# Performance work log

Hardware: AMD Instinct MI355X
Metric: run time of the kernel (lower is better)

Reference implementation:

```python
import jax, jax.numpy as jnp
import numpy as np


def setup_inputs() -> dict:
    key = jax.random.key(0)
    k1, k2 = jax.random.split(key)
    # x: (batch=16, channels=256, window=64, n_patches=128)
    x = jax.random.normal(k1, (16, 256, 64, 128), dtype=jnp.float32)
    # codebooks: (nsubq=4, codebook_size=2**(num_bits//2)=256, sub_channels=64)
    codebooks = jax.random.normal(k2, (4, 256, 64), dtype=jnp.float32)
    return {"x": x, "codebooks": codebooks}


def reference(x, codebooks):
    B, C, W, P = x.shape
    ns, K, sc = codebooks.shape  # ns=4, K=256, sc=C//ns
    # split channels into nsubq subspaces: (B, ns, sc, W, P) -> (ns, B*W*P, sc)
    xs = x.reshape(B, ns, sc, W, P).transpose(1, 0, 3, 4, 2).reshape(ns, B * W * P, sc)
    # squared euclidean distances (argmin identical to cdist argmin)
    d2 = (jnp.sum(xs * xs, axis=-1, keepdims=True)
          - 2.0 * jnp.einsum('snc,skc->snk', xs, codebooks)
          + jnp.sum(codebooks * codebooks, axis=-1)[:, None, :])  # (ns, N, K)
    idx = jnp.argmin(d2, axis=-1)  # (ns, N)
    q = jnp.take_along_axis(codebooks, idx[:, :, None], axis=1)  # (ns, N, sc)
    # faithful to the torch code: data was flattened in (B, W, P) order but
    # view()'d back as (B, P, W) -- reshape reproduces that reinterpretation
    q = q.reshape(ns, B, P, W, sc).transpose(1, 2, 3, 0, 4).reshape(B, P, W, C)
    # final permute(0, 3, 2, 1) -> (B, C, W, P)
    return q.transpose(0, 3, 2, 1)
```

## Files before the change

### kernel.cpp

```cpp
#include <hip/hip_runtime.h>

#define NSQ 4
#define KCB 256
#define SCH 64
#define NVEC (16*64*128)

__global__ void pq_norms(const float* __restrict__ cb, float* __restrict__ cn)
{
    const int s = blockIdx.x, k = threadIdx.x;
    const float* row = cb + (size_t)(s * KCB + k) * SCH;
    float n = 0.f;
#pragma unroll
    for (int j4 = 0; j4 < 16; ++j4) {
        float4 v = *(const float4*)(row + j4 * 4);
        n = fmaf(v.x, v.x, n); n = fmaf(v.y, v.y, n);
        n = fmaf(v.z, v.z, n); n = fmaf(v.w, v.w, n);
    }
    cn[s * KCB + k] = n;
}

__global__ __launch_bounds__(512, 2) void pq_pass1(const float* __restrict__ x,
                                                   const float* __restrict__ cb,
                                                   const float* __restrict__ cnorm,
                                                   int* __restrict__ idx_out)
{
    __shared__ float cbt[64][256];
    const int tid = threadIdx.x;
    const int s   = blockIdx.x >> 7;
    const int blk = blockIdx.x & 127;
    const int tk  = tid & 15;
    const int tn  = tid >> 4;
    const int swz = ((tk ^ (tk >> 2)) & 3) << 2;

    if (tid < 256) {
        const int k    = tid;
        const int tks  = k >> 4;
        const int szs  = ((tks ^ (tks >> 2)) & 3) << 2;
        const int col  = (k & ~15) | ((k & 15) ^ szs);
        const float* row = cb + (size_t)(s * KCB + k) * SCH;
#pragma unroll
        for (int j4 = 0; j4 < 16; ++j4) {
            float4 v = *(const float4*)(row + j4 * 4);
            cbt[j4*4 + 0][col] = v.x;
            cbt[j4*4 + 1][col] = v.y;
            cbt[j4*4 + 2][col] = v.z;
            cbt[j4*4 + 3][col] = v.w;
        }
    }
    __syncthreads();

    const int cb0 = (tk << 4) | (0  ^ swz);
    const int cb1 = (tk << 4) | (4  ^ swz);
    const int cb2 = (tk << 4) | (8  ^ swz);
    const int cb3 = (tk << 4) | (12 ^ swz);
    const float* cnp = cnorm + s * KCB + (tk << 4);

    int n_base = blk * 1024;
    const float* xp = x + ((size_t)(((n_base >> 13) * 256 + s * 64) * 64 +
                                    ((n_base >> 7) & 63))) * 128 + 4 * tn;
    float4 xv = *(const float4*)xp;

    for (int t = 0; t < 8; ++t) {
        float acc[4][16];
#pragma unroll
        for (int nn = 0; nn < 4; ++nn)
#pragma unroll
            for (int kk = 0; kk < 16; ++kk) acc[nn][kk] = 0.f;

#pragma unroll 2
        for (int j = 0; j < 63; ++j) {
            float4 xn = *(const float4*)(xp + (size_t)(j + 1) * 8192);
            float c[16];
            {
                float4 t0 = *(const float4*)&cbt[j][cb0];
                float4 t1 = *(const float4*)&cbt[j][cb1];
                float4 t2 = *(const float4*)&cbt[j][cb2];
                float4 t3 = *(const float4*)&cbt[j][cb3];
                c[0]=t0.x; c[1]=t0.y; c[2]=t0.z; c[3]=t0.w;
                c[4]=t1.x; c[5]=t1.y; c[6]=t1.z; c[7]=t1.w;
                c[8]=t2.x; c[9]=t2.y; c[10]=t2.z; c[11]=t2.w;
                c[12]=t3.x; c[13]=t3.y; c[14]=t3.z; c[15]=t3.w;
            }
#pragma unroll
            for (int kk = 0; kk < 16; ++kk) {
                acc[0][kk] = fmaf(xv.x, c[kk], acc[0][kk]);
                acc[1][kk] = fmaf(xv.y, c[kk], acc[1][kk]);
                acc[2][kk] = fmaf(xv.z, c[kk], acc[2][kk]);
                acc[3][kk] = fmaf(xv.w, c[kk], acc[3][kk]);
            }
            xv = xn;
        }
        {
            const int nb2 = blk * 1024 + (t < 7 ? (t + 1) : t) * 128;
            const float* xp2 = x + ((size_t)(((nb2 >> 13) * 256 + s * 64) * 64 +
                                             ((nb2 >> 7) & 63))) * 128 + 4 * tn;
            float4 xnext = *(const float4*)xp2;

            float c[16];
            {
                float4 t0 = *(const float4*)&cbt[63][cb0];
                float4 t1 = *(const float4*)&cbt[63][cb1];
                float4 t2 = *(const float4*)&cbt[63][cb2];
                float4 t3 = *(const float4*)&cbt[63][cb3];
                c[0]=t0.x; c[1]=t0.y; c[2]=t0.z; c[3]=t0.w;
                c[4]=t1.x; c[5]=t1.y; c[6]=t1.z; c[7]=t1.w;
                c[8]=t2.x; c[9]=t2.y; c[10]=t2.z; c[11]=t2.w;
                c[12]=t3.x; c[13]=t3.y; c[14]=t3.z; c[15]=t3.w;
            }
#pragma unroll
            for (int kk = 0; kk < 16; ++kk) {
                acc[0][kk] = fmaf(xv.x, c[kk], acc[0][kk]);
                acc[1][kk] = fmaf(xv.y, c[kk], acc[1][kk]);
                acc[2][kk] = fmaf(xv.z, c[kk], acc[2][kk]);
                acc[3][kk] = fmaf(xv.w, c[kk], acc[3][kk]);
            }
            xv = xnext;
            xp = xp2;
        }

        float best[4] = {3.4e38f, 3.4e38f, 3.4e38f, 3.4e38f};
        int   bidx[4] = {0, 0, 0, 0};
#pragma unroll
        for (int kk = 0; kk < 16; ++kk) {
            const float cn = cnp[kk];
            const int k = (tk << 4) + kk;
#pragma unroll
            for (int nn = 0; nn < 4; ++nn) {
                float d = fmaf(-2.f, acc[nn][kk], cn);
                bool better = (d < best[nn]);
                best[nn] = better ? d : best[nn];
                bidx[nn] = better ? k : bidx[nn];
            }
        }
#pragma unroll
        for (int m = 8; m; m >>= 1) {
#pragma unroll
            for (int nn = 0; nn < 4; ++nn) {
                float ob = __shfl_xor(best[nn], m, 64);
                int   oi = __shfl_xor(bidx[nn], m, 64);
                bool take = (ob < best[nn]) || (ob == best[nn] && oi < bidx[nn]);
                best[nn] = take ? ob : best[nn];
                bidx[nn] = take ? oi : bidx[nn];
            }
        }
        if (tk == 0) {
            int4 r; r.x = bidx[0]; r.y = bidx[1]; r.z = bidx[2]; r.w = bidx[3];
            *(int4*)(idx_out + (size_t)s * NVEC + n_base + 4 * tn) = r;
        }
        n_base += 128;
    }
}

__global__ __launch_bounds__(256) void pq_pass2(const float* __restrict__ cb,
                                                const int* __restrict__ idx,
                                                float* __restrict__ out)
{
    __shared__ int   L[64][65];
    __shared__ float cbs[256][9];
    const int tid = threadIdx.x;
    const int bid = blockIdx.x;
    const int jq  = bid & 7;
    const int ph  = (bid >> 3) & 1;
    const int s   = (bid >> 4) & 3;
    const int b   = bid >> 6;
    const int p0  = ph * 64;
    const int j0  = jq * 8;

    const int* ip = idx + (size_t)s * NVEC + b * 8192 + p0 * 64;
#pragma unroll
    for (int it = 0; it < 16; ++it) {
        int g = it * 256 + tid;
        L[g & 63][g >> 6] = ip[g];
    }
    const float* cp = cb + (size_t)s * (KCB * SCH) + j0;
#pragma unroll
    for (int it = 0; it < 2; ++it) {
        int t = it * 256 + tid;
        int k = t >> 1, jj4 = (t & 1) * 4;
        float4 v = *(const float4*)(cp + (size_t)k * SCH + jj4);
        cbs[k][jj4 + 0] = v.x; cbs[k][jj4 + 1] = v.y;
        cbs[k][jj4 + 2] = v.z; cbs[k][jj4 + 3] = v.w;
    }
    __syncthreads();

    int kv[4][4];
#pragma unroll
    for (int q = 0; q < 4; ++q) {
        int ch = q * 256 + tid;
        int w  = ch >> 4, pp = (ch & 15) * 4;
#pragma unroll
        for (int e = 0; e < 4; ++e) kv[q][e] = L[w][pp + e];
    }

#pragma unroll
    for (int cc = 0; cc < 8; ++cc) {
        const int c = s * 64 + j0 + cc;
        float* op = out + ((size_t)(b * 256 + c) * 64) * 128 + p0;
#pragma unroll
        for (int q = 0; q < 4; ++q) {
            int ch = q * 256 + tid;
            int w  = ch >> 4, pp = (ch & 15) * 4;
            float4 v;
            v.x = cbs[kv[q][0]][cc];
            v.y = cbs[kv[q][1]][cc];
            v.z = cbs[kv[q][2]][cc];
            v.w = cbs[kv[q][3]][cc];
            *(float4*)(op + (size_t)w * 128 + pp) = v;
        }
    }
}

extern "C" void kernel_launch(void* const* d_in, const int* in_sizes, int n_in,
                              void* d_out, int out_size, void* d_ws, size_t ws_size,
                              hipStream_t stream) {
    (void)in_sizes; (void)n_in; (void)out_size; (void)ws_size;
    const float* x   = (const float*)d_in[0];
    const float* cbk = (const float*)d_in[1];
    float*       out = (float*)d_out;
    int*         idx = (int*)d_ws;
    float*       cnrm = (float*)d_out;

    pq_norms<<<NSQ, KCB, 0, stream>>>(cbk, cnrm);
    pq_pass1<<<NSQ * 128, 512, 0, stream>>>(x, cbk, cnrm, idx);
    pq_pass2<<<16 * NSQ * 2 * 8, 256, 0, stream>>>(cbk, idx, out);
}
```

Measured before the change: 545.3 us.

## Split pass1 into many small blocks with chunked codebook staging in LDS

The distance kernel moves from 512 persistent-style blocks, each covering 1024 vectors with the full 64x256 codebook in LDS, to 8192 blocks of 256 threads covering 64 vectors each. The codebook is now staged in four 16-row chunks separated by barriers, so LDS per block drops from 64 KB to 16 KB and more blocks can be resident per CU. The goal is better occupancy and load balance across the GPU. In exchange, every block reloads the whole codebook from global or L2 memory and pays extra barriers, and the amortization of codebook staging across 8 tiles is lost.

```diff
diff --git a/kernel.cpp b/kernel.cpp
--- a/kernel.cpp
+++ b/kernel.cpp
@@ -19,35 +19,29 @@
     cn[s * KCB + k] = n;
 }
 
-__global__ __launch_bounds__(512, 2) void pq_pass1(const float* __restrict__ x,
+__global__ __launch_bounds__(256, 4) void pq_pass1(const float* __restrict__ x,
                                                    const float* __restrict__ cb,
                                                    const float* __restrict__ cnorm,
                                                    int* __restrict__ idx_out)
 {
-    __shared__ float cbt[64][256];
-    const int tid = threadIdx.x;
-    const int s   = blockIdx.x >> 7;
-    const int blk = blockIdx.x & 127;
-    const int tk  = tid & 15;
-    const int tn  = tid >> 4;
-    const int swz = ((tk ^ (tk >> 2)) & 3) << 2;
-
-    if (tid < 256) {
-        const int k    = tid;
-        const int tks  = k >> 4;
-        const int szs  = ((tks ^ (tks >> 2)) & 3) << 2;
-        const int col  = (k & ~15) | ((k & 15) ^ szs);
-        const float* row = cb + (size_t)(s * KCB + k) * SCH;
-#pragma unroll
-        for (int j4 = 0; j4 < 16; ++j4) {
-            float4 v = *(const float4*)(row + j4 * 4);
-            cbt[j4*4 + 0][col] = v.x;
-            cbt[j4*4 + 1][col] = v.y;
-            cbt[j4*4 + 2][col] = v.z;
-            cbt[j4*4 + 3][col] = v.w;
-        }
-    }
-    __syncthreads();
+    __shared__ float cbt[16][256];
+    const int tid  = threadIdx.x;
+    const int s    = blockIdx.x >> 11;
+    const int blkn = blockIdx.x & 2047;
+    const int tk   = tid & 15;
+    const int tn   = tid >> 4;
+    const int swz  = ((tk ^ (tk >> 2)) & 3) << 2;
+
+    const int n_base = blkn * 64;
+    const int b   = n_base >> 13;
+    const int w   = (n_base >> 7) & 63;
+    const int p0  = n_base & 127;
+
+    const int k    = tid;
+    const int tks  = k >> 4;
+    const int szs  = ((tks ^ (tks >> 2)) & 3) << 2;
+    const int col  = (k & ~15) | ((k & 15) ^ szs);
+    const float* cbrow = cb + (size_t)(s * KCB + k) * SCH;
 
     const int cb0 = (tk << 4) | (0  ^ swz);
     const int cb1 = (tk << 4) | (4  ^ swz);
@@ -55,27 +49,41 @@
     const int cb3 = (tk << 4) | (12 ^ swz);
     const float* cnp = cnorm + s * KCB + (tk << 4);
 
-    int n_base = blk * 1024;
-    const float* xp = x + ((size_t)(((n_base >> 13) * 256 + s * 64) * 64 +
-                                    ((n_base >> 7) & 63))) * 128 + 4 * tn;
+    const float* xp = x + ((size_t)((b * 256 + s * 64) * 64 + w)) * 128 + p0 + 4 * tn;
     float4 xv = *(const float4*)xp;
 
-    for (int t = 0; t < 8; ++t) {
-        float acc[4][16];
-#pragma unroll
-        for (int nn = 0; nn < 4; ++nn)
-#pragma unroll
-            for (int kk = 0; kk < 16; ++kk) acc[nn][kk] = 0.f;
-
-#pragma unroll 2
-        for (int j = 0; j < 63; ++j) {
-            float4 xn = *(const float4*)(xp + (size_t)(j + 1) * 8192);
+    float acc[4][16];
+#pragma unroll
+    for (int nn = 0; nn < 4; ++nn)
+#pragma unroll
+        for (int kk = 0; kk < 16; ++kk) acc[nn][kk] = 0.f;
+
+    for (int ch = 0; ch < 4; ++ch) {
+        __syncthreads();
+        {
+            const float* rp = cbrow + ch * 16;
+            float4 v0 = *(const float4*)(rp + 0);
+            float4 v1 = *(const float4*)(rp + 4);
+            float4 v2 = *(const float4*)(rp + 8);
+            float4 v3 = *(const float4*)(rp + 12);
+            cbt[ 0][col] = v0.x; cbt[ 1][col] = v0.y; cbt[ 2][col] = v0.z; cbt[ 3][col] = v0.w;
+            cbt[ 4][col] = v1.x; cbt[ 5][col] = v1.y; cbt[ 6][col] = v1.z; cbt[ 7][col] = v1.w;
+            cbt[ 8][col] = v2.x; cbt[ 9][col] = v2.y; cbt[10][col] = v2.z; cbt[11][col] = v2.w;
+            cbt[12][col] = v3.x; cbt[13][col] = v3.y; cbt[14][col] = v3.z; cbt[15][col] = v3.w;
+        }
+        __syncthreads();
+
+#pragma unroll
+        for (int jj = 0; jj < 16; ++jj) {
+            const int j  = ch * 16 + jj;
+            const int jn = (j < 63) ? (j + 1) : 63;
+            float4 xn = *(const float4*)(xp + (size_t)jn * 8192);
             float c[16];
             {
-                float4 t0 = *(const float4*)&cbt[j][cb0];
-                float4 t1 = *(const float4*)&cbt[j][cb1];
-                float4 t2 = *(const float4*)&cbt[j][cb2];
-                float4 t3 = *(const float4*)&cbt[j][cb3];
+                float4 t0 = *(const float4*)&cbt[jj][cb0];
+                float4 t1 = *(const float4*)&cbt[jj][cb1];
+                float4 t2 = *(const float4*)&cbt[jj][cb2];
+                float4 t3 = *(const float4*)&cbt[jj][cb3];
                 c[0]=t0.x; c[1]=t0.y; c[2]=t0.z; c[3]=t0.w;
                 c[4]=t1.x; c[5]=t1.y; c[6]=t1.z; c[7]=t1.w;
                 c[8]=t2.x; c[9]=t2.y; c[10]=t2.z; c[11]=t2.w;
@@ -90,64 +98,36 @@
             }
             xv = xn;
         }
-        {
-            const int nb2 = blk * 1024 + (t < 7 ? (t + 1) : t) * 128;
-            const float* xp2 = x + ((size_t)(((nb2 >> 13) * 256 + s * 64) * 64 +
-                                             ((nb2 >> 7) & 63))) * 128 + 4 * tn;
-            float4 xnext = *(const float4*)xp2;
-
-            float c[16];
-            {
-                float4 t0 = *(const float4*)&cbt[63][cb0];
-                float4 t1 = *(const float4*)&cbt[63][cb1];
-                float4 t2 = *(const float4*)&cbt[63][cb2];
-                float4 t3 = *(const float4*)&cbt[63][cb3];
-                c[0]=t0.x; c[1]=t0.y; c[2]=t0.z; c[3]=t0.w;
-                c[4]=t1.x; c[5]=t1.y; c[6]=t1.z; c[7]=t1.w;
-                c[8]=t2.x; c[9]=t2.y; c[10]=t2.z; c[11]=t2.w;
-                c[12]=t3.x; c[13]=t3.y; c[14]=t3.z; c[15]=t3.w;
-            }
-#pragma unroll
-            for (int kk = 0; kk < 16; ++kk) {
-                acc[0][kk] = fmaf(xv.x, c[kk], acc[0][kk]);
-                acc[1][kk] = fmaf(xv.y, c[kk], acc[1][kk]);
-                acc[2][kk] = fmaf(xv.z, c[kk], acc[2][kk]);
-                acc[3][kk] = fmaf(xv.w, c[kk], acc[3][kk]);
-            }
-            xv = xnext;
-            xp = xp2;
-        }
-
-        float best[4] = {3.4e38f, 3.4e38f, 3.4e38f, 3.4e38f};
-        int   bidx[4] = {0, 0, 0, 0};
-#pragma unroll
-        for (int kk = 0; kk < 16; ++kk) {
-            const float cn = cnp[kk];
-            const int k = (tk << 4) + kk;
-#pragma unroll
-            for (int nn = 0; nn < 4; ++nn) {
-                float d = fmaf(-2.f, acc[nn][kk], cn);
-                bool better = (d < best[nn]);
-                best[nn] = better ? d : best[nn];
-                bidx[nn] = better ? k : bidx[nn];
-            }
-        }
-#pragma unroll
-        for (int m = 8; m; m >>= 1) {
-#pragma unroll
-            for (int nn = 0; nn < 4; ++nn) {
-                float ob = __shfl_xor(best[nn], m, 64);
-                int   oi = __shfl_xor(bidx[nn], m, 64);
-                bool take = (ob < best[nn]) || (ob == best[nn] && oi < bidx[nn]);
-                best[nn] = take ? ob : best[nn];
-                bidx[nn] = take ? oi : bidx[nn];
-            }
-        }
-        if (tk == 0) {
-            int4 r; r.x = bidx[0]; r.y = bidx[1]; r.z = bidx[2]; r.w = bidx[3];
-            *(int4*)(idx_out + (size_t)s * NVEC + n_base + 4 * tn) = r;
-        }
-        n_base += 128;
+    }
+
+    float best[4] = {3.4e38f, 3.4e38f, 3.4e38f, 3.4e38f};
+    int   bidx[4] = {0, 0, 0, 0};
+#pragma unroll
+    for (int kk = 0; kk < 16; ++kk) {
+        const float cn = cnp[kk];
+        const int kx = (tk << 4) + kk;
+#pragma unroll
+        for (int nn = 0; nn < 4; ++nn) {
+            float d = fmaf(-2.f, acc[nn][kk], cn);
+            bool better = (d < best[nn]);
+            best[nn] = better ? d : best[nn];
+            bidx[nn] = better ? kx : bidx[nn];
+        }
+    }
+#pragma unroll
+    for (int m = 8; m; m >>= 1) {
+#pragma unroll
+        for (int nn = 0; nn < 4; ++nn) {
+            float ob = __shfl_xor(best[nn], m, 64);
+            int   oi = __shfl_xor(bidx[nn], m, 64);
+            bool take = (ob < best[nn]) || (ob == best[nn] && oi < bidx[nn]);
+            best[nn] = take ? ob : best[nn];
+            bidx[nn] = take ? oi : bidx[nn];
+        }
+    }
+    if (tk == 0) {
+        int4 r; r.x = bidx[0]; r.y = bidx[1]; r.z = bidx[2]; r.w = bidx[3];
+        *(int4*)(idx_out + (size_t)s * NVEC + n_base + 4 * tn) = r;
     }
 }
 
@@ -221,6 +201,6 @@
     float*       cnrm = (float*)d_out;
 
     pq_norms<<<NSQ, KCB, 0, stream>>>(cbk, cnrm);
-    pq_pass1<<<NSQ * 128, 512, 0, stream>>>(x, cbk, cnrm, idx);
+    pq_pass1<<<NSQ * 2048, 256, 0, stream>>>(x, cbk, cnrm, idx);
     pq_pass2<<<16 * NSQ * 2 * 8, 256, 0, stream>>>(cbk, idx, out);
 }
```

Measured after the change: 640.8 us. 17.5% more time.
